# Optimization experiments

Measured on AMD Instinct MI355X. Metric: run time of the kernel, lower is better.

Reference implementation:

```python
import jax, jax.numpy as jnp
import numpy as np

B, S, HID = 2, 2048, 2048
NH, HD = 16, 128            # num heads, head dim (HID = NH*HD)
ROT = 64                    # rotary_dim
MASK_VALUE = -10000.0


def _rotate_every_two(x):
    # x: [..., d] with d even; interleaved (-x2, x1)
    x1 = x[..., ::2]
    x2 = x[..., 1::2]
    return jnp.stack((-x2, x1), axis=-1).reshape(x.shape)


def _fixed_sincos(seq_len, dim):
    inv_freq = 1.0 / (10000.0 ** (jnp.arange(0, dim, 2, dtype=jnp.float32) / dim))
    t = jnp.arange(seq_len, dtype=jnp.float32)
    ang = t[:, None] * inv_freq[None, :]          # [S, dim/2]
    return jnp.sin(ang), jnp.cos(ang)


def _apply_rope(x, sin, cos):
    # x: [B, S, H, rot]; sin/cos: [S, rot/2] -> repeat_interleave(2) -> [S, rot]
    sin = jnp.repeat(sin, 2, axis=-1)[None, :, None, :]
    cos = jnp.repeat(cos, 2, axis=-1)[None, :, None, :]
    return x * cos + _rotate_every_two(x) * sin


def setup_inputs() -> dict:
    key = jax.random.key(0)
    ks = jax.random.split(key, 7)
    w_scale = 1.0 / np.sqrt(HID)
    return {
        "hidden_states": jax.random.normal(ks[0], (B, S, HID), dtype=jnp.float32),
        "attention_mask": jnp.zeros((B, 1, 1, S), dtype=jnp.float32),
        "Wq": jax.random.normal(ks[1], (HID, HID), dtype=jnp.float32) * w_scale,
        "bq": jnp.zeros((HID,), dtype=jnp.float32),
        "Wk": jax.random.normal(ks[2], (HID, HID), dtype=jnp.float32) * w_scale,
        "bk": jnp.zeros((HID,), dtype=jnp.float32),
        "Wv": jax.random.normal(ks[3], (HID, HID), dtype=jnp.float32) * w_scale,
        "bv": jnp.zeros((HID,), dtype=jnp.float32),
    }


def reference(hidden_states, attention_mask, Wq, bq, Wk, bk, Wv, bv):
    # QKV projections (torch Linear: x @ W.T + b)
    q = (hidden_states @ Wq.T + bq).reshape(B, S, NH, HD)
    k = (hidden_states @ Wk.T + bk).reshape(B, S, NH, HD)
    v = (hidden_states @ Wv.T + bv).reshape(B, S, NH, HD)

    # Inline rotary on first ROT dims of q/k
    sin, cos = _fixed_sincos(S, ROT)
    q = jnp.concatenate([_apply_rope(q[..., :ROT], sin, cos), q[..., ROT:]], axis=-1)
    k = jnp.concatenate([_apply_rope(k[..., :ROT], sin, cos), k[..., ROT:]], axis=-1)

    # Scores [B, H, S, S]
    scores = jnp.einsum('bqhd,bkhd->bhqk', q, k) / np.sqrt(HD)

    # Causal mask + additive attention mask
    causal = jnp.tril(jnp.ones((S, S), dtype=bool))[None, None]
    scores = jnp.where(causal, scores, jnp.asarray(MASK_VALUE, scores.dtype))
    scores = scores + attention_mask

    probs = jax.nn.softmax(scores, axis=-1)
    ctx = jnp.einsum('bhqk,bkhd->bqhd', probs, v)
    return ctx.reshape(B, S, HID)
```

## Files before the change

### kernel.cpp

```cpp
#include <hip/hip_runtime.h>

typedef unsigned short bhalf;
typedef __attribute__((ext_vector_type(4))) float    f32x4;
typedef __attribute__((ext_vector_type(8))) short    s16x8;
typedef __attribute__((ext_vector_type(4))) float    floatx4;
typedef __attribute__((ext_vector_type(4))) unsigned short u16x4;

#define B_  2
#define S_  2048
#define HID_ 2048
#define NH_ 16
#define HD_ 128
#define M_  (B_*S_)
#define MASKV (-10000.0f)

__device__ __forceinline__ bhalf f32_to_bf16(float f) {
    union { float f; unsigned int u; } v; v.f = f;
    unsigned int r = v.u + 0x7FFFu + ((v.u >> 16) & 1u);
    return (bhalf)(r >> 16);
}
__device__ __forceinline__ bhalf f32_to_bf16_trunc(float f) {
    union { float f; unsigned int u; } v; v.f = f;
    return (bhalf)(v.u >> 16);
}
__device__ __forceinline__ float bf16_to_f32(bhalf h) {
    union { unsigned int u; float f; } v; v.u = ((unsigned int)h) << 16;
    return v.f;
}

__device__ __forceinline__ void gl_lds16(const void* g, void* l) {
    __builtin_amdgcn_global_load_lds(
        (const __attribute__((address_space(1))) void*)g,
        (__attribute__((address_space(3))) void*)l, 16, 0, 0);
}

#define BARRIER() asm volatile("s_barrier" ::: "memory")

__global__ __launch_bounds__(256) void cast_all(const float* __restrict__ hs,
                                                const float* __restrict__ Wq,
                                                const float* __restrict__ Wk,
                                                const float* __restrict__ Wv,
                                                bhalf* __restrict__ dst) {
    int idx = blockIdx.x * 256 + threadIdx.x;
    const float* src;
    if (idx < 2097152)      src = hs + (size_t)idx * 4;
    else if (idx < 3145728) src = Wq + (size_t)(idx - 2097152) * 4;
    else if (idx < 4194304) src = Wk + (size_t)(idx - 3145728) * 4;
    else                    src = Wv + (size_t)(idx - 4194304) * 4;
    floatx4 f = *(const floatx4*)src;
    u16x4 o;
    o.x = f32_to_bf16(f.x); o.y = f32_to_bf16(f.y);
    o.z = f32_to_bf16(f.z); o.w = f32_to_bf16(f.w);
    *(u16x4*)(dst + (size_t)idx * 4) = o;
}

__global__ __launch_bounds__(512, 2) void qkv_gemm(const bhalf* __restrict__ A,
                                                   const bhalf* __restrict__ Wb,
                                                   const float* __restrict__ bq,
                                                   const float* __restrict__ bk,
                                                   const float* __restrict__ bv,
                                                   bhalf* __restrict__ Out,
                                                   bhalf* __restrict__ VTo) {
    __shared__ __align__(16) bhalf As[2][16384];
    __shared__ __align__(16) bhalf Bs[2][16384];
    const int tid  = threadIdx.x;
    const int lane = tid & 63, w = tid >> 6;
    const int quad = lane >> 4, l = lane & 15;
    const int wy = w >> 2, wx = w & 3;
    const int m0 = blockIdx.x * 256, n0 = blockIdx.y * 256;
    const int z  = blockIdx.z;
    const bhalf* W    = Wb + (size_t)z * HID_ * HID_;
    const float* bias = (z == 0) ? bq : (z == 1) ? bk : bv;
    bhalf* out        = Out + (size_t)z * M_ * HID_;

    bhalf* AsF = &As[0][0];
    bhalf* BsF = &Bs[0][0];

    const int row_s = tid >> 3;
    const int kg_s  = (tid & 7) ^ (row_s & 7);
    const int w512  = w * 512;

    const bhalf* gA0 = A + (size_t)(m0 +   0 + row_s) * HID_ + kg_s * 8;
    const bhalf* gA1 = A + (size_t)(m0 +  64 + row_s) * HID_ + kg_s * 8;
    const bhalf* gA2 = A + (size_t)(m0 + 128 + row_s) * HID_ + kg_s * 8;
    const bhalf* gA3 = A + (size_t)(m0 + 192 + row_s) * HID_ + kg_s * 8;
    const bhalf* gB0 = W + (size_t)(n0 +   0 + row_s) * HID_ + kg_s * 8;
    const bhalf* gB1 = W + (size_t)(n0 +  64 + row_s) * HID_ + kg_s * 8;
    const bhalf* gB2 = W + (size_t)(n0 + 128 + row_s) * HID_ + kg_s * 8;
    const bhalf* gB3 = W + (size_t)(n0 + 192 + row_s) * HID_ + kg_s * 8;

    const int aIdx = (wy * 128 + l) * 64;
    const int bIdx = (wx * 64  + l) * 64;
    const int swz0 = ((0 + quad) ^ (l & 7)) * 8;
    const int swz1 = ((4 + quad) ^ (l & 7)) * 8;

    f32x4 acc[8][4] = {};

#define ADV() do { gA0 += 64; gA1 += 64; gA2 += 64; gA3 += 64;               \
                   gB0 += 64; gB1 += 64; gB2 += 64; gB3 += 64; } while (0)

#define KTILE(BUF, ST1, ST2, VM) do {                                        \
    const int CB = (BUF) * 16384, NB = ((BUF) ^ 1) * 16384;                  \
    s16x8 a_[4][2], b01_[2][2], b23_[2][2];                                  \
                    \
    _Pragma("unroll") for (int mt = 0; mt < 4; ++mt) {                       \
        a_[mt][0] = *(const s16x8*)(AsF + CB + aIdx + mt * 1024 + swz0);     \
        a_[mt][1] = *(const s16x8*)(AsF + CB + aIdx + mt * 1024 + swz1); }   \
    _Pragma("unroll") for (int nt = 0; nt < 2; ++nt) {                       \
        b01_[nt][0] = *(const s16x8*)(BsF + CB + bIdx + nt * 1024 + swz0);   \
        b01_[nt][1] = *(const s16x8*)(BsF + CB + bIdx + nt * 1024 + swz1); } \
    if (ST1) { gl_lds16(gA1 + 64, AsF + NB + 1 * 4096 + w512);               \
               gl_lds16(gA3 + 64, AsF + NB + 3 * 4096 + w512); }             \
    BARRIER();                                                               \
    __builtin_amdgcn_s_setprio(1);                                           \
    _Pragma("unroll") for (int mt = 0; mt < 4; ++mt)                         \
      _Pragma("unroll") for (int nt = 0; nt < 2; ++nt)                       \
        _Pragma("unroll") for (int ks = 0; ks < 2; ++ks)                     \
          acc[mt][nt] = __builtin_amdgcn_mfma_f32_16x16x32_bf16(             \
              a_[mt][ks], b01_[nt][ks], acc[mt][nt], 0, 0, 0);               \
    __builtin_amdgcn_s_setprio(0);                                           \
    BARRIER();                                                               \
                           \
    _Pragma("unroll") for (int nt = 0; nt < 2; ++nt) {                       \
        b23_[nt][0] = *(const s16x8*)(BsF + CB + bIdx + (nt+2)*1024 + swz0); \
        b23_[nt][1] = *(const s16x8*)(BsF + CB + bIdx + (nt+2)*1024 + swz1);}\
    if (ST2) { gl_lds16(gA0 + 128, AsF + CB + 0 * 4096 + w512);              \
               gl_lds16(gA2 + 128, AsF + CB + 2 * 4096 + w512); }            \
    BARRIER();                                                               \
    __builtin_amdgcn_s_setprio(1);                                           \
    _Pragma("unroll") for (int mt = 0; mt < 4; ++mt)                         \
      _Pragma("unroll") for (int nt = 0; nt < 2; ++nt)                       \
        _Pragma("unroll") for (int ks = 0; ks < 2; ++ks)                     \
          acc[mt][nt + 2] = __builtin_amdgcn_mfma_f32_16x16x32_bf16(         \
              a_[mt][ks], b23_[nt][ks], acc[mt][nt + 2], 0, 0, 0);           \
    __builtin_amdgcn_s_setprio(0);                                           \
    BARRIER();                                                               \
                        \
    _Pragma("unroll") for (int mt = 0; mt < 4; ++mt) {                       \
        a_[mt][0] = *(const s16x8*)(AsF + CB + aIdx + 4096 + mt*1024 + swz0);\
        a_[mt][1] = *(const s16x8*)(AsF + CB + aIdx + 4096 + mt*1024 + swz1);}\
    if (ST2) { gl_lds16(gB0 + 128, BsF + CB + 0 * 4096 + w512);              \
               gl_lds16(gB1 + 128, BsF + CB + 1 * 4096 + w512); }            \
    BARRIER();                                                               \
    __builtin_amdgcn_s_setprio(1);                                           \
    _Pragma("unroll") for (int mt = 0; mt < 4; ++mt)                         \
      _Pragma("unroll") for (int nt = 0; nt < 2; ++nt)                       \
        _Pragma("unroll") for (int ks = 0; ks < 2; ++ks)                     \
          acc[4 + mt][nt + 2] = __builtin_amdgcn_mfma_f32_16x16x32_bf16(     \
              a_[mt][ks], b23_[nt][ks], acc[4 + mt][nt + 2], 0, 0, 0);       \
    __builtin_amdgcn_s_setprio(0);                                           \
    BARRIER();                                                               \
    \
    if (ST2) { gl_lds16(gB2 + 128, BsF + CB + 2 * 4096 + w512);              \
               gl_lds16(gB3 + 128, BsF + CB + 3 * 4096 + w512); }            \
    if ((VM) == 6)      asm volatile("s_waitcnt vmcnt(6)" ::: "memory");     \
    else if ((VM) == 0) asm volatile("s_waitcnt vmcnt(0)" ::: "memory");     \
    BARRIER();                                                               \
    __builtin_amdgcn_s_setprio(1);                                           \
    _Pragma("unroll") for (int mt = 0; mt < 4; ++mt)                         \
      _Pragma("unroll") for (int nt = 0; nt < 2; ++nt)                       \
        _Pragma("unroll") for (int ks = 0; ks < 2; ++ks)                     \
          acc[4 + mt][nt] = __builtin_amdgcn_mfma_f32_16x16x32_bf16(         \
              a_[mt][ks], b01_[nt][ks], acc[4 + mt][nt], 0, 0, 0);           \
    __builtin_amdgcn_s_setprio(0);                                           \
    BARRIER();                                                               \
} while (0)

    gl_lds16(gA0, AsF + 0 * 4096 + w512);
    gl_lds16(gA2, AsF + 2 * 4096 + w512);
    gl_lds16(gB0, BsF + 0 * 4096 + w512);
    gl_lds16(gB1, BsF + 1 * 4096 + w512);
    gl_lds16(gB2, BsF + 2 * 4096 + w512);
    gl_lds16(gB3, BsF + 3 * 4096 + w512);
    gl_lds16(gA1, AsF + 1 * 4096 + w512);
    gl_lds16(gA3, AsF + 3 * 4096 + w512);
    gl_lds16(gA0 + 64, AsF + 16384 + 0 * 4096 + w512);
    gl_lds16(gA2 + 64, AsF + 16384 + 2 * 4096 + w512);
    gl_lds16(gB0 + 64, BsF + 16384 + 0 * 4096 + w512);
    gl_lds16(gB1 + 64, BsF + 16384 + 1 * 4096 + w512);
    gl_lds16(gB2 + 64, BsF + 16384 + 2 * 4096 + w512);
    gl_lds16(gB3 + 64, BsF + 16384 + 3 * 4096 + w512);
    asm volatile("s_waitcnt vmcnt(6)" ::: "memory");
    BARRIER();

    for (int tt = 0; tt < 15; ++tt) {
        KTILE(0, 1, 1, 6); ADV();
        KTILE(1, 1, 1, 6); ADV();
    }
    KTILE(0, 1, 0, 0); ADV();
    KTILE(1, 0, 0, -1);

#undef KTILE
#undef ADV

    if (z == 2) {
#pragma unroll
        for (int mt = 0; mt < 8; ++mt) {
#pragma unroll
            for (int nt = 0; nt < 4; ++nt) {
                int col = n0 + wx * 64 + nt * 16 + l;
                float bv_ = bias[col];
                int row0 = m0 + wy * 128 + mt * 16 + quad * 4;
                int bb = row0 >> 11, s0 = row0 & 2047;
                u16x4 o;
#pragma unroll
                for (int r = 0; r < 4; ++r) o[r] = f32_to_bf16(acc[mt][nt][r] + bv_);
                *(u16x4*)(VTo + ((size_t)(bb * 16) * 128 + col) * S_ + s0) = o;
            }
        }
    } else {
#pragma unroll
        for (int mt = 0; mt < 8; ++mt) {
#pragma unroll
            for (int nt = 0; nt < 4; ++nt) {
                int col = n0 + wx * 64 + nt * 16 + l;
                float bv_ = bias[col];
#pragma unroll
                for (int r = 0; r < 4; ++r) {
                    int row = m0 + wy * 128 + mt * 16 + quad * 4 + r;
                    out[(size_t)row * HID_ + col] = f32_to_bf16(acc[mt][nt][r] + bv_);
                }
            }
        }
    }
}

__global__ __launch_bounds__(256) void rope_table(float2* __restrict__ tab) {
    int idx = blockIdx.x * 256 + threadIdx.x;
    int i = idx & 31, s = idx >> 5;
    float inv = expf(-(float)i * 0.2878231366242557f);
    float ang = (float)s * inv;
    tab[idx] = make_float2(sinf(ang), cosf(ang));
}

__global__ __launch_bounds__(256) void rope_apply(bhalf* __restrict__ Qb,
                                                  bhalf* __restrict__ Kb,
                                                  const float2* __restrict__ tab) {
    int flat = blockIdx.x * 256 + threadIdx.x;
    int i = flat & 31;
    int h = (flat >> 5) & 15;
    int s = (flat >> 9) & 2047;
    int b = flat >> 20;
    size_t base = ((size_t)(b * S_ + s)) * HID_ + h * HD_ + 2 * i;
    float2 sc = tab[s * 32 + i];
    float c = sc.y, sn = sc.x;
    {
        unsigned int q = *(const unsigned int*)(Qb + base);
        float x0 = bf16_to_f32((bhalf)(q & 0xffff));
        float x1 = bf16_to_f32((bhalf)(q >> 16));
        unsigned int o = (unsigned int)f32_to_bf16(x0 * c - x1 * sn)
                       | ((unsigned int)f32_to_bf16(x1 * c + x0 * sn) << 16);
        *(unsigned int*)(Qb + base) = o;
    }
    {
        unsigned int k = *(const unsigned int*)(Kb + base);
        float x0 = bf16_to_f32((bhalf)(k & 0xffff));
        float x1 = bf16_to_f32((bhalf)(k >> 16));
        unsigned int o = (unsigned int)f32_to_bf16(x0 * c - x1 * sn)
                       | ((unsigned int)f32_to_bf16(x1 * c + x0 * sn) << 16);
        *(unsigned int*)(Kb + base) = o;
    }
}

__global__ __launch_bounds__(512, 2) void flash_attn(const bhalf* __restrict__ Qb,
                                                     const bhalf* __restrict__ Kb,
                                                     const bhalf* __restrict__ VT,
                                                     const float* __restrict__ amask,
                                                     float* __restrict__ out) {
    __shared__ __align__(16) bhalf Kbuf[2][2048 * 8];
    __shared__ __align__(16) bhalf Vbuf[2][2048 * 8];
    const int tid = threadIdx.x, lane = tid & 63, w = tid >> 6;
    const int quad = lane >> 4, l = lane & 15;
    const int qt = blockIdx.x, bh = blockIdx.y;
    const int b = bh >> 4, h = bh & 15;
    const bool is_hi = (w < 4);
    const int ws = w & 3;
    const int myrow = is_hi ? ((31 - qt) * 64 + ws * 16) : (qt * 64 + ws * 16);
    const int ch_hi   = (33 - qt) >> 1;
    const int lo_last = (qt * 64 + 63) >> 7;
    const int my_last = is_hi ? (ch_hi - 1) : lo_last;

    s16x8 qf[4];
    {
        const bhalf* Qrow = Qb + (size_t)(b * S_ + myrow + l) * HID_ + h * HD_;
#pragma unroll
        for (int ks = 0; ks < 4; ++ks)
            qf[ks] = *(const s16x8*)(Qrow + ks * 32 + quad * 8);
    }
    s16x8 ones;
#pragma unroll
    for (int j = 0; j < 8; ++j) ones[j] = (short)0x3F80;

    float m_run[4] = {-1e30f, -1e30f, -1e30f, -1e30f};
    f32x4 l_acc = {};
    f32x4 acc[8] = {};
    const int fpl = ((l >> 2) << 1) | (l & 1);

#pragma unroll
    for (int j = 0; j < 4; ++j) {
        int slot0 = j * 512 + w * 64;
        int slot  = slot0 + lane;
        int row = slot >> 4, x = slot & 15;
        int g   = (x & 8) | ((x ^ row) & 7);
        gl_lds16(Kb + (size_t)(b * S_ + row) * HID_ + h * HD_ + g * 8,
                 &Kbuf[0][slot0 * 8]);
        gl_lds16(VT + ((size_t)bh * HD_ + row) * S_ + g * 8,
                 &Vbuf[0][slot0 * 8]);
    }

    for (int kc = 0; kc < ch_hi; ++kc) {
        const int cur = kc & 1, nxt = cur ^ 1;
        const int key0 = kc * 128;
        __syncthreads();

        const bool active = (kc <= my_last);
        const bool diag   = (kc == my_last);

        float am[8];
        if (active) {
#pragma unroll
            for (int nt = 0; nt < 8; ++nt) am[nt] = amask[b * S_ + key0 + nt * 16 + l];
        }
        if (kc + 1 < ch_hi) {
            const int key1 = key0 + 128;
#pragma unroll
            for (int j = 0; j < 4; ++j) {
                int slot0 = j * 512 + w * 64;
                int slot  = slot0 + lane;
                int row = slot >> 4, x = slot & 15;
                int g   = (x & 8) | ((x ^ row) & 7);
                gl_lds16(Kb + (size_t)(b * S_ + key1 + row) * HID_ + h * HD_ + g * 8,
                         &Kbuf[nxt][slot0 * 8]);
                gl_lds16(VT + ((size_t)bh * HD_ + row) * S_ + key1 + g * 8,
                         &Vbuf[nxt][slot0 * 8]);
            }
        }

        const bhalf* Kc = &Kbuf[cur][0];
        const bhalf* Vc = &Vbuf[cur][0];
        bhalf* Pw = &Kbuf[cur][0] + w * 2048;

        f32x4 s[8] = {};
        if (active) {
#pragma unroll
            for (int nt = 0; nt < 8; ++nt) {
                int key = nt * 16 + l;
#pragma unroll
                for (int ks = 0; ks < 4; ++ks) {
                    int dg = ks * 4 + quad;
                    int x  = (dg & 8) | ((dg ^ key) & 7);
                    s16x8 kf = *(const s16x8*)(Kc + (key * 16 + x) * 8);
                    s[nt] = __builtin_amdgcn_mfma_f32_16x16x32_bf16(qf[ks], kf, s[nt], 0, 0, 0);
                }
            }
        }
        __asm__ __volatile__("s_waitcnt lgkmcnt(0)\n\ts_barrier" ::: "memory");

        if (active) {
#pragma unroll
            for (int r = 0; r < 4; ++r) {
                const int qrow = myrow + quad * 4 + r;
                float p[8];
#pragma unroll
                for (int nt = 0; nt < 8; ++nt) {
                    float v = s[nt][r] * 0.08838834764831845f;
                    if (diag) { int key = key0 + nt * 16 + l; v = (key > qrow) ? MASKV : v; }
                    p[nt] = v + am[nt];
                }
                float mx = fmaxf(fmaxf(fmaxf(p[0], p[1]), fmaxf(p[2], p[3])),
                                 fmaxf(fmaxf(p[4], p[5]), fmaxf(p[6], p[7])));
#pragma unroll
                for (int msk = 1; msk < 16; msk <<= 1) mx = fmaxf(mx, __shfl_xor(mx, msk, 64));
                float m_new = fmaxf(m_run[r], mx);
                float alpha = __expf(m_run[r] - m_new);
                m_run[r] = m_new;
                const int m  = quad * 4 + r;
                const int fm = (quad << 1) | (r & 1);
#pragma unroll
                for (int nt = 0; nt < 8; ++nt) {
                    float e = __expf(p[nt] - m_new);
                    int key = nt * 16 + l;
                    Pw[(m * 16 + ((key >> 3) ^ fm)) * 8 + (key & 7)] = f32_to_bf16_trunc(e);
                }
                l_acc[r] *= alpha;
#pragma unroll
                for (int nt = 0; nt < 8; ++nt) acc[nt][r] *= alpha;
            }
#pragma unroll
            for (int kstep = 0; kstep < 4; ++kstep) {
                int kg = kstep * 4 + quad;
                s16x8 pf = *(const s16x8*)(Pw + (l * 16 + (kg ^ fpl)) * 8);
                l_acc = __builtin_amdgcn_mfma_f32_16x16x32_bf16(pf, ones, l_acc, 0, 0, 0);
#pragma unroll
                for (int nt = 0; nt < 8; ++nt) {
                    int d = nt * 16 + l;
                    int x = (kg & 8) | ((kg ^ d) & 7);
                    s16x8 vf = *(const s16x8*)(Vc + (d * 16 + x) * 8);
                    acc[nt] = __builtin_amdgcn_mfma_f32_16x16x32_bf16(pf, vf, acc[nt], 0, 0, 0);
                }
            }
        }
    }

    float inv[4];
#pragma unroll
    for (int r = 0; r < 4; ++r) inv[r] = 1.f / l_acc[r];
#pragma unroll
    for (int nt = 0; nt < 8; ++nt) {
        int col = h * HD_ + nt * 16 + l;
#pragma unroll
        for (int r = 0; r < 4; ++r)
            out[(size_t)(b * S_ + myrow + quad * 4 + r) * HID_ + col] = acc[nt][r] * inv[r];
    }
}

extern "C" void kernel_launch(void* const* d_in, const int* in_sizes, int n_in,
                              void* d_out, int out_size, void* d_ws, size_t ws_size,
                              hipStream_t stream) {
    const float* hs    = (const float*)d_in[0];
    const float* amask = (const float*)d_in[1];
    const float* Wq    = (const float*)d_in[2];
    const float* bq    = (const float*)d_in[3];
    const float* Wk    = (const float*)d_in[4];
    const float* bk    = (const float*)d_in[5];
    const float* Wv    = (const float*)d_in[6];
    const float* bv    = (const float*)d_in[7];
    float* out = (float*)d_out;

    bhalf* hsb = (bhalf*)d_ws;
    bhalf* wqb = hsb + 8388608;
    bhalf* wkb = wqb + 4194304;
    bhalf* wvb = wkb + 4194304;
    bhalf* Qb  = wvb + 4194304;
    bhalf* Kb  = Qb + 8388608;
    bhalf* VTb = Kb + 8388608;
    float2* tab = (float2*)(VTb + 8388608);

    rope_table<<<256, 256, 0, stream>>>(tab);
    cast_all<<<20480, 256, 0, stream>>>(hs, Wq, Wk, Wv, hsb);
    qkv_gemm<<<dim3(16, 8, 3), 512, 0, stream>>>(hsb, wqb, bq, bk, bv, Qb, VTb);
    rope_apply<<<8192, 256, 0, stream>>>(Qb, Kb, tab);
    flash_attn<<<dim3(16, 32), 512, 0, stream>>>(Qb, Kb, VTb, amask, out);
}
```

Measured before the change: 361.9 us.

## Remap block IDs for XCD-aware L2 locality and restage A tile loads

```diff
diff --git a/kernel.cpp b/kernel.cpp
--- a/kernel.cpp
+++ b/kernel.cpp
@@ -67,8 +67,14 @@
     const int lane = tid & 63, w = tid >> 6;
     const int quad = lane >> 4, l = lane & 15;
     const int wy = w >> 2, wx = w & 3;
-    const int m0 = blockIdx.x * 256, n0 = blockIdx.y * 256;
-    const int z  = blockIdx.z;
+
+    const int f  = blockIdx.x + 16 * blockIdx.y + 128 * blockIdx.z;
+    const int L  = (f & 7) * 48 + (f >> 3);
+    const int z  = L >> 7;
+    const int by = (L >> 4) & 7;
+    const int bx = L & 15;
+    const int m0 = bx * 256, n0 = by * 256;
+
     const bhalf* W    = Wb + (size_t)z * HID_ * HID_;
     const float* bias = (z == 0) ? bq : (z == 1) ? bk : bv;
     bhalf* out        = Out + (size_t)z * M_ * HID_;
@@ -99,18 +105,16 @@
 #define ADV() do { gA0 += 64; gA1 += 64; gA2 += 64; gA3 += 64;               \
                    gB0 += 64; gB1 += 64; gB2 += 64; gB3 += 64; } while (0)
 
-#define KTILE(BUF, ST1, ST2, VM) do {                                        \
-    const int CB = (BUF) * 16384, NB = ((BUF) ^ 1) * 16384;                  \
+#define KTILE(BUF, ST2, VM) do {                                             \
+    const int CB = (BUF) * 16384;                                            \
     s16x8 a_[4][2], b01_[2][2], b23_[2][2];                                  \
-                    \
+                             \
     _Pragma("unroll") for (int mt = 0; mt < 4; ++mt) {                       \
         a_[mt][0] = *(const s16x8*)(AsF + CB + aIdx + mt * 1024 + swz0);     \
         a_[mt][1] = *(const s16x8*)(AsF + CB + aIdx + mt * 1024 + swz1); }   \
     _Pragma("unroll") for (int nt = 0; nt < 2; ++nt) {                       \
         b01_[nt][0] = *(const s16x8*)(BsF + CB + bIdx + nt * 1024 + swz0);   \
         b01_[nt][1] = *(const s16x8*)(BsF + CB + bIdx + nt * 1024 + swz1); } \
-    if (ST1) { gl_lds16(gA1 + 64, AsF + NB + 1 * 4096 + w512);               \
-               gl_lds16(gA3 + 64, AsF + NB + 3 * 4096 + w512); }             \
     BARRIER();                                                               \
     __builtin_amdgcn_s_setprio(1);                                           \
     _Pragma("unroll") for (int mt = 0; mt < 4; ++mt)                         \
@@ -120,7 +124,7 @@
               a_[mt][ks], b01_[nt][ks], acc[mt][nt], 0, 0, 0);               \
     __builtin_amdgcn_s_setprio(0);                                           \
     BARRIER();                                                               \
-                           \
+          \
     _Pragma("unroll") for (int nt = 0; nt < 2; ++nt) {                       \
         b23_[nt][0] = *(const s16x8*)(BsF + CB + bIdx + (nt+2)*1024 + swz0); \
         b23_[nt][1] = *(const s16x8*)(BsF + CB + bIdx + (nt+2)*1024 + swz1);}\
@@ -135,7 +139,7 @@
               a_[mt][ks], b23_[nt][ks], acc[mt][nt + 2], 0, 0, 0);           \
     __builtin_amdgcn_s_setprio(0);                                           \
     BARRIER();                                                               \
-                        \
+      \
     _Pragma("unroll") for (int mt = 0; mt < 4; ++mt) {                       \
         a_[mt][0] = *(const s16x8*)(AsF + CB + aIdx + 4096 + mt*1024 + swz0);\
         a_[mt][1] = *(const s16x8*)(AsF + CB + aIdx + 4096 + mt*1024 + swz1);}\
@@ -150,10 +154,12 @@
               a_[mt][ks], b23_[nt][ks], acc[4 + mt][nt + 2], 0, 0, 0);       \
     __builtin_amdgcn_s_setprio(0);                                           \
     BARRIER();                                                               \
-    \
-    if (ST2) { gl_lds16(gB2 + 128, BsF + CB + 2 * 4096 + w512);              \
+                   \
+    if (ST2) { gl_lds16(gA1 + 128, AsF + CB + 1 * 4096 + w512);              \
+               gl_lds16(gA3 + 128, AsF + CB + 3 * 4096 + w512);              \
+               gl_lds16(gB2 + 128, BsF + CB + 2 * 4096 + w512);              \
                gl_lds16(gB3 + 128, BsF + CB + 3 * 4096 + w512); }            \
-    if ((VM) == 6)      asm volatile("s_waitcnt vmcnt(6)" ::: "memory");     \
+    if ((VM) == 8)      asm volatile("s_waitcnt vmcnt(8)" ::: "memory");     \
     else if ((VM) == 0) asm volatile("s_waitcnt vmcnt(0)" ::: "memory");     \
     BARRIER();                                                               \
     __builtin_amdgcn_s_setprio(1);                                           \
@@ -167,28 +173,30 @@
 } while (0)
 
     gl_lds16(gA0, AsF + 0 * 4096 + w512);
+    gl_lds16(gA1, AsF + 1 * 4096 + w512);
     gl_lds16(gA2, AsF + 2 * 4096 + w512);
+    gl_lds16(gA3, AsF + 3 * 4096 + w512);
     gl_lds16(gB0, BsF + 0 * 4096 + w512);
     gl_lds16(gB1, BsF + 1 * 4096 + w512);
     gl_lds16(gB2, BsF + 2 * 4096 + w512);
     gl_lds16(gB3, BsF + 3 * 4096 + w512);
-    gl_lds16(gA1, AsF + 1 * 4096 + w512);
-    gl_lds16(gA3, AsF + 3 * 4096 + w512);
     gl_lds16(gA0 + 64, AsF + 16384 + 0 * 4096 + w512);
+    gl_lds16(gA1 + 64, AsF + 16384 + 1 * 4096 + w512);
     gl_lds16(gA2 + 64, AsF + 16384 + 2 * 4096 + w512);
+    gl_lds16(gA3 + 64, AsF + 16384 + 3 * 4096 + w512);
     gl_lds16(gB0 + 64, BsF + 16384 + 0 * 4096 + w512);
     gl_lds16(gB1 + 64, BsF + 16384 + 1 * 4096 + w512);
     gl_lds16(gB2 + 64, BsF + 16384 + 2 * 4096 + w512);
     gl_lds16(gB3 + 64, BsF + 16384 + 3 * 4096 + w512);
-    asm volatile("s_waitcnt vmcnt(6)" ::: "memory");
+    asm volatile("s_waitcnt vmcnt(8)" ::: "memory");
     BARRIER();
 
     for (int tt = 0; tt < 15; ++tt) {
-        KTILE(0, 1, 1, 6); ADV();
-        KTILE(1, 1, 1, 6); ADV();
-    }
-    KTILE(0, 1, 0, 0); ADV();
-    KTILE(1, 0, 0, -1);
+        KTILE(0, 1, 8); ADV();
+        KTILE(1, 1, 8); ADV();
+    }
+    KTILE(0, 0, 0); ADV();
+    KTILE(1, 0, -1);
 
 #undef KTILE
 #undef ADV
@@ -271,7 +279,9 @@
     __shared__ __align__(16) bhalf Vbuf[2][2048 * 8];
     const int tid = threadIdx.x, lane = tid & 63, w = tid >> 6;
     const int quad = lane >> 4, l = lane & 15;
-    const int qt = blockIdx.x, bh = blockIdx.y;
+    const int f  = blockIdx.x + 16 * blockIdx.y;
+    const int Lf = (f & 7) * 64 + (f >> 3);
+    const int qt = Lf & 15, bh = Lf >> 4;
     const int b = bh >> 4, h = bh & 15;
     const bool is_hi = (w < 4);
     const int ws = w & 3;
```

After: 377.2 us. +4.2%, slower.
